# Performance work log

Measured on AMD Instinct MI355X. Metric: run time of the kernel, lower is better.

Reference implementation:

```python
import jax, jax.numpy as jnp
import numpy as np

D_MODEL = 1024
N_HEAD = 16
SEG = 256
HEAD_DIM = D_MODEL // N_HEAD  # 64; only used as softmax scale (module never splits heads)
SCALE = 1.0 / (HEAD_DIM ** 0.5)


def setup_inputs() -> dict:
    key = jax.random.key(0)
    ks = jax.random.split(key, 9)
    B, L, D = 4, 4096, D_MODEL
    s = 1.0 / np.sqrt(D)
    x = jax.random.normal(ks[0], (B, L, D), dtype=jnp.float32)
    Wq = jax.random.uniform(ks[1], (D, D), jnp.float32, -s, s)
    bq = jax.random.uniform(ks[2], (D,), jnp.float32, -s, s)
    Wk = jax.random.uniform(ks[3], (D, D), jnp.float32, -s, s)
    bk = jax.random.uniform(ks[4], (D,), jnp.float32, -s, s)
    Wv = jax.random.uniform(ks[5], (D, D), jnp.float32, -s, s)
    bv = jax.random.uniform(ks[6], (D,), jnp.float32, -s, s)
    Wo = jax.random.uniform(ks[7], (D, D), jnp.float32, -s, s)
    bo = jax.random.uniform(ks[8], (D,), jnp.float32, -s, s)
    return {"x": x, "Wq": Wq, "bq": bq, "Wk": Wk, "bk": bk,
            "Wv": Wv, "bv": bv, "Wo": Wo, "bo": bo}


def reference(x, Wq, bq, Wk, bk, Wv, bv, Wo, bo):
    B, L, D = x.shape
    n_seg = L // SEG
    xs = x.reshape(B, n_seg, SEG, D)  # [B, n, S, D] block-diagonal segments

    # Local (per-segment) attention, batched over all segments at once.
    Q = jnp.einsum('bnsd,ed->bnse', xs, Wq) + bq
    K = jnp.einsum('bnsd,ed->bnse', xs, Wk) + bk
    V = jnp.einsum('bnsd,ed->bnse', xs, Wv) + bv
    scores = jnp.einsum('bnse,bnte->bnst', Q, K) * SCALE  # [B, n, S, S]
    attn = jax.nn.softmax(scores, axis=-1)
    local = jnp.einsum('bnst,bnte->bnse', attn, V)  # [B, n, S, D]

    # Global attention over segment summaries (first token of each segment).
    summ = xs[:, :, 0, :]  # [B, n, D]
    Qg = jnp.einsum('bnd,ed->bne', summ, Wq) + bq
    Kg = jnp.einsum('bnd,ed->bne', summ, Wk) + bk
    Vg = jnp.einsum('bnd,ed->bne', summ, Wv) + bv
    scores_g = jnp.einsum('bne,bme->bnm', Qg, Kg) * SCALE  # [B, n, n]
    attn_g = jax.nn.softmax(scores_g, axis=-1)
    global_out = jnp.einsum('bnm,bme->bne', attn_g, Vg)  # [B, n, D]

    # Broadcast each segment's global summary over its tokens and add.
    out = local + global_out[:, :, None, :]  # [B, n, S, D]
    out = out.reshape(B, L, D)
    return jnp.einsum('bld,ed->ble', out, Wo) + bo
```

## Files before the change

### kernel.cpp

```cpp
#include <hip/hip_runtime.h>
#include <hip/hip_bf16.h>
#include <stdint.h>

typedef unsigned short u16;
typedef __attribute__((ext_vector_type(8))) short s16x8;
typedef __attribute__((ext_vector_type(4))) short s16x4;
typedef __attribute__((ext_vector_type(4))) float f32x4;

__device__ __forceinline__ u16 f2bf(float f){
  uint32_t u = __builtin_bit_cast(uint32_t, f);
  u += 0x7FFFu + ((u >> 16) & 1u);
  return (u16)(u >> 16);
}
__device__ __forceinline__ float bf2f(u16 h){
  uint32_t u = ((uint32_t)h) << 16;
  return __builtin_bit_cast(float, u);
}
__device__ __forceinline__ void gl_lds16(const void* g, void* l){
  __builtin_amdgcn_global_load_lds((__attribute__((address_space(1))) void*)g,
                                   (__attribute__((address_space(3))) void*)l,
                                   16, 0, 0);
}

#define MROWS 16384
#define DMODEL 1024
#define NQKV 3072
#define NSEGS 64
#define O_XB    0u
#define O_WQKV  33554432u
#define O_WO    39845888u
#define O_BQKV  41943040u
#define O_QKV   41955328u
#define O_VT    142618624u
#define O_GOUT  176173056u
#define O_GPR   176435200u

__global__ __launch_bounds__(256) void pack_kernel(
    const float* __restrict__ x,
    const float* __restrict__ wq, const float* __restrict__ wk,
    const float* __restrict__ wv, const float* __restrict__ wo,
    const float* __restrict__ bq, const float* __restrict__ bk, const float* __restrict__ bv,
    u16* __restrict__ xb, u16* __restrict__ wqkvb, u16* __restrict__ wob,
    float* __restrict__ bqkv)
{
  const int stride = gridDim.x * 256;
  const int gid = blockIdx.x * 256 + threadIdx.x;
  if(gid < 3072)
    bqkv[gid] = (gid < 1024) ? bq[gid] : (gid < 2048 ? bk[gid - 1024] : bv[gid - 2048]);
  for(int q = gid; q < 4194304; q += stride){
    float4 v = *(const float4*)(x + (size_t)q * 4);
    ushort4 o; o.x = f2bf(v.x); o.y = f2bf(v.y); o.z = f2bf(v.z); o.w = f2bf(v.w);
    *(ushort4*)(xb + (size_t)q * 4) = o;
  }
  for(int q = gid; q < 786432; q += stride){
    int elem = q << 2;
    int m = elem >> 20;
    const float* s = (m == 0) ? wq : (m == 1 ? wk : wv);
    float4 v = *(const float4*)(s + (elem & 1048575));
    ushort4 o; o.x = f2bf(v.x); o.y = f2bf(v.y); o.z = f2bf(v.z); o.w = f2bf(v.w);
    *(ushort4*)(wqkvb + elem) = o;
  }
  for(int q = gid; q < 262144; q += stride){
    float4 v = *(const float4*)(wo + (size_t)q * 4);
    ushort4 o; o.x = f2bf(v.x); o.y = f2bf(v.y); o.z = f2bf(v.z); o.w = f2bf(v.w);
    *(ushort4*)(wob + (size_t)q * 4) = o;
  }
}

__global__ __launch_bounds__(512, 2) void gemm256_kernel(
    const u16* __restrict__ A, const u16* __restrict__ Bt,
    const float* __restrict__ bias, u16* __restrict__ Cv,
    u16* __restrict__ Vt, const int K, const int ldc, const int ncb)
{
  __shared__ char sm[131072];
  const int tid = threadIdx.x;
  const int wv = tid >> 6, lane = tid & 63;
  const int l15 = lane & 15, l4 = lane >> 4;
  const int wr = wv >> 2, wc = wv & 3;

  const int nwg = (int)gridDim.x;
  int bid = (int)blockIdx.x;
  bid = (bid & 7) * (nwg >> 3) + (bid >> 3);
  const int brow = (bid / ncb) << 8, bcol = (bid % ncb) << 8;

  int offA[8], offB[4];
#pragma unroll
  for(int m = 0; m < 8; ++m){
    int row = wr * 128 + m * 16 + l15;
    offA[m] = row * 64 + ((l4 ^ ((row >> 1) & 3)) << 4);
  }
#pragma unroll
  for(int n = 0; n < 4; ++n){
    int row = wc * 64 + n * 16 + l15;
    offB[n] = 16384 + row * 64 + ((l4 ^ ((row >> 1) & 3)) << 4);
  }

  const u16* srcA[2]; const u16* srcB[2]; int dstOff[2];
#pragma unroll
  for(int r = 0; r < 2; ++r){
    int off = r * 8192 + tid * 16;
    int row = off >> 6, g = (off >> 4) & 3;
    int gs = g ^ ((row >> 1) & 3);
    srcA[r] = A  + (size_t)(brow + row) * K + gs * 8;
    srcB[r] = Bt + (size_t)(bcol + row) * K + gs * 8;
    dstOff[r] = r * 8192 + wv * 1024;
  }

#define STAGE256(kt_, buf_) do{                                   \
    char* base_ = sm + (buf_) * 32768;                            \
    const int ko_ = (kt_) << 5;                                   \
    gl_lds16(srcA[0] + ko_, base_ + dstOff[0]);                   \
    gl_lds16(srcA[1] + ko_, base_ + dstOff[1]);                   \
    gl_lds16(srcB[0] + ko_, base_ + 16384 + dstOff[0]);           \
    gl_lds16(srcB[1] + ko_, base_ + 16384 + dstOff[1]);           \
  }while(0)

  const f32x4 fz = {0.f, 0.f, 0.f, 0.f};
  f32x4 acc[8][4];
#pragma unroll
  for(int m = 0; m < 8; ++m)
#pragma unroll
    for(int n = 0; n < 4; ++n) acc[m][n] = fz;

  const int nkt = K >> 5;
  STAGE256(0, 0); STAGE256(1, 1); STAGE256(2, 2);

  for(int kt = 0; kt < nkt; ++kt){
    const int rem = nkt - 1 - kt;
    if(rem >= 2)      asm volatile("s_waitcnt vmcnt(8)" ::: "memory");
    else if(rem == 1) asm volatile("s_waitcnt vmcnt(4)" ::: "memory");
    else              asm volatile("s_waitcnt vmcnt(0)" ::: "memory");
    __builtin_amdgcn_s_barrier();
    asm volatile("" ::: "memory");
    if(kt + 3 < nkt) STAGE256(kt + 3, (kt + 3) & 3);

    char* cb = sm + (kt & 3) * 32768;
    s16x8 b[4], a[4];
#pragma unroll
    for(int n = 0; n < 4; ++n) b[n] = *(const s16x8*)(cb + offB[n]);
#pragma unroll
    for(int m = 0; m < 4; ++m) a[m] = *(const s16x8*)(cb + offA[m]);
    __builtin_amdgcn_s_setprio(1);
#pragma unroll
    for(int m = 0; m < 4; ++m)
#pragma unroll
      for(int n = 0; n < 4; ++n)
        acc[m][n] = __builtin_amdgcn_mfma_f32_16x16x32_bf16(a[m], b[n], acc[m][n], 0, 0, 0);
    __builtin_amdgcn_s_setprio(0);
#pragma unroll
    for(int m = 0; m < 4; ++m) a[m] = *(const s16x8*)(cb + offA[m + 4]);
    __builtin_amdgcn_s_setprio(1);
#pragma unroll
    for(int m = 0; m < 4; ++m)
#pragma unroll
      for(int n = 0; n < 4; ++n)
        acc[m + 4][n] = __builtin_amdgcn_mfma_f32_16x16x32_bf16(a[m], b[n], acc[m + 4][n], 0, 0, 0);
    __builtin_amdgcn_s_setprio(0);
  }
#undef STAGE256

  float bvv[4];
#pragma unroll
  for(int n = 0; n < 4; ++n) bvv[n] = bias[bcol + wc * 64 + n * 16 + l15];

  if(bcol < 2048){
#pragma unroll
    for(int m = 0; m < 8; ++m)
#pragma unroll
      for(int n = 0; n < 4; ++n)
#pragma unroll
        for(int r = 0; r < 4; ++r){
          const int row = brow + wr * 128 + m * 16 + (l4 << 2) + r;
          const int col = bcol + wc * 64 + n * 16 + l15;
          Cv[(size_t)row * ldc + col] = f2bf(acc[m][n][r] + bvv[n]);
        }
  } else {
    __syncthreads();
    char* wbase = sm + wv * 16384;
    const int swzW = (l15 & 7) << 4;
#pragma unroll
    for(int n = 0; n < 4; ++n)
#pragma unroll
      for(int m = 0; m < 8; ++m){
        s16x4 pk;
#pragma unroll
        for(int r = 0; r < 4; ++r) pk[r] = (short)f2bf(acc[m][n][r] + bvv[n]);
        const int eL = n * 16 + l15;
        const int tB = (m * 16 + (l4 << 2)) * 2;
        *(s16x4*)(wbase + ((eL * 256 + tB) ^ swzW)) = pk;
      }
    asm volatile("s_waitcnt lgkmcnt(0)" ::: "memory");
    const int seg = brow >> 8;
    const int e0  = bcol - 2048 + wc * 64;
    const int c = lane & 15, eSub = lane >> 4;
#pragma unroll
    for(int i = 0; i < 16; ++i){
      const int eL = i * 4 + eSub;
      s16x8 vvv = *(const s16x8*)(wbase + ((eL * 256 + c * 16) ^ ((eL & 7) << 4)));
      *(s16x8*)(Vt + (size_t)seg * 262144 + (size_t)(e0 + eL) * 256 + wr * 128 + c * 8) = vvv;
    }
  }
}

__global__ __launch_bounds__(512, 4) void gemm128_kernel(
    const u16* __restrict__ A, const u16* __restrict__ Bt,
    const float* __restrict__ bias, float* __restrict__ C,
    const int K, const int ldc, const int ncb)
{
  __shared__ char sm[73728];
  const int tid = threadIdx.x;
  const int wv = tid >> 6, lane = tid & 63;
  const int l15 = lane & 15, l4 = lane >> 4;
  const int wr = wv >> 2, wc = wv & 3;

  const int nwg = (int)gridDim.x;
  int bid = (int)blockIdx.x;
  bid = (bid & 7) * (nwg >> 3) + (bid >> 3);
  const int brow = (bid / ncb) << 8, bcol = (bid % ncb) << 7;

  int offA[8], offB[2];
#pragma unroll
  for(int m = 0; m < 8; ++m){
    int row = wr * 128 + m * 16 + l15;
    offA[m] = row * 64 + ((l4 ^ ((row >> 1) & 3)) << 4);
  }
#pragma unroll
  for(int n = 0; n < 2; ++n){
    int row = wc * 32 + n * 16 + l15;
    offB[n] = 16384 + row * 64 + ((l4 ^ ((row >> 1) & 3)) << 4);
  }

  const u16* srcA[2]; const u16* srcB; int dstOff[2];
#pragma unroll
  for(int r = 0; r < 2; ++r){
    int off = r * 8192 + tid * 16;
    int row = off >> 6, g = (off >> 4) & 3;
    int gs = g ^ ((row >> 1) & 3);
    srcA[r] = A + (size_t)(brow + row) * K + gs * 8;
    dstOff[r] = r * 8192 + wv * 1024;
  }
  {
    int off = tid * 16;
    int row = off >> 6, g = (off >> 4) & 3;
    int gs = g ^ ((row >> 1) & 3);
    srcB = Bt + (size_t)(bcol + row) * K + gs * 8;
  }

#define STAGE128(kt_, buf_) do{                                   \
    char* base_ = sm + (buf_) * 24576;                            \
    const int ko_ = (kt_) << 5;                                   \
    gl_lds16(srcA[0] + ko_, base_ + dstOff[0]);                   \
    gl_lds16(srcA[1] + ko_, base_ + dstOff[1]);                   \
    gl_lds16(srcB + ko_, base_ + 16384 + wv * 1024);              \
  }while(0)

  const f32x4 fz = {0.f, 0.f, 0.f, 0.f};
  f32x4 acc[8][2];
#pragma unroll
  for(int m = 0; m < 8; ++m)
#pragma unroll
    for(int n = 0; n < 2; ++n) acc[m][n] = fz;

  const int nkt = K >> 5;
  STAGE128(0, 0); STAGE128(1, 1);
  int cur = 0;
  for(int kt = 0; kt < nkt; ++kt){
    if(kt + 1 < nkt) asm volatile("s_waitcnt vmcnt(3)" ::: "memory");
    else             asm volatile("s_waitcnt vmcnt(0)" ::: "memory");
    __builtin_amdgcn_s_barrier();
    asm volatile("" ::: "memory");
    if(kt + 2 < nkt){
      int nb = cur + 2; if(nb >= 3) nb -= 3;
      STAGE128(kt + 2, nb);
    }
    char* cb = sm + cur * 24576;
    s16x8 b[2], a[4];
#pragma unroll
    for(int n = 0; n < 2; ++n) b[n] = *(const s16x8*)(cb + offB[n]);
#pragma unroll
    for(int m = 0; m < 4; ++m) a[m] = *(const s16x8*)(cb + offA[m]);
    __builtin_amdgcn_s_setprio(1);
#pragma unroll
    for(int m = 0; m < 4; ++m)
#pragma unroll
      for(int n = 0; n < 2; ++n)
        acc[m][n] = __builtin_amdgcn_mfma_f32_16x16x32_bf16(a[m], b[n], acc[m][n], 0, 0, 0);
    __builtin_amdgcn_s_setprio(0);
#pragma unroll
    for(int m = 0; m < 4; ++m) a[m] = *(const s16x8*)(cb + offA[m + 4]);
    __builtin_amdgcn_s_setprio(1);
#pragma unroll
    for(int m = 0; m < 4; ++m)
#pragma unroll
      for(int n = 0; n < 2; ++n)
        acc[m + 4][n] = __builtin_amdgcn_mfma_f32_16x16x32_bf16(a[m], b[n], acc[m + 4][n], 0, 0, 0);
    __builtin_amdgcn_s_setprio(0);
    if(++cur == 3) cur = 0;
  }
#undef STAGE128

  float bvv[2];
#pragma unroll
  for(int n = 0; n < 2; ++n) bvv[n] = bias[bcol + wc * 32 + n * 16 + l15];
#pragma unroll
  for(int m = 0; m < 8; ++m)
#pragma unroll
    for(int n = 0; n < 2; ++n)
#pragma unroll
      for(int r = 0; r < 4; ++r){
        const int row = brow + wr * 128 + m * 16 + (l4 << 2) + r;
        const int col = bcol + wc * 32 + n * 16 + l15;
        C[(size_t)row * ldc + col] = acc[m][n][r] + bvv[n];
      }
}

__global__ __launch_bounds__(256) void gscore_kernel(
    const u16* __restrict__ QKV, float* __restrict__ gpr)
{
  __shared__ float sc[16];
  const int b = blockIdx.x >> 4, i = blockIdx.x & 15;
  const int tid = threadIdx.x;
  const int j = tid >> 4, slice = tid & 15;
  const u16* qp = QKV + (size_t)(b * 16 + i) * 256 * NQKV + slice * 64;
  const u16* kp = QKV + (size_t)(b * 16 + j) * 256 * NQKV + 1024 + slice * 64;
  float acc = 0.f;
#pragma unroll
  for(int c = 0; c < 8; ++c){
    s16x8 qv = *(const s16x8*)(qp + c * 8);
    s16x8 kv = *(const s16x8*)(kp + c * 8);
#pragma unroll
    for(int e = 0; e < 8; ++e) acc += bf2f((u16)qv[e]) * bf2f((u16)kv[e]);
  }
#pragma unroll
  for(int off = 8; off >= 1; off >>= 1) acc += __shfl_xor(acc, off, 64);
  if(slice == 0) sc[j] = acc * 0.125f;
  __syncthreads();
  if(tid < 16){
    float v = sc[tid];
    float m = v;
#pragma unroll
    for(int off = 8; off >= 1; off >>= 1) m = fmaxf(m, __shfl_xor(m, off, 64));
    float p = __expf(v - m);
    float s = p;
#pragma unroll
    for(int off = 8; off >= 1; off >>= 1) s += __shfl_xor(s, off, 64);
    gpr[(size_t)b * 256 + i * 16 + tid] = p / s;
  }
}

__global__ __launch_bounds__(256) void gpv_kernel(
    const u16* __restrict__ Vt, const float* __restrict__ gpr,
    float* __restrict__ gout)
{
  __shared__ float spr[256];
  const int b = blockIdx.x >> 4, ch = blockIdx.x & 15;
  const int tid = threadIdx.x;
  spr[tid] = gpr[(size_t)b * 256 + tid];
  __syncthreads();
  const int e = (ch << 6) + (tid & 63);
  const int ng = tid >> 6;
  const u16* vp = Vt + (size_t)(b * 16) * 262144 + (size_t)e * 256;
  float o0 = 0.f, o1 = 0.f, o2 = 0.f, o3 = 0.f;
#pragma unroll
  for(int m = 0; m < 16; ++m){
    float v = bf2f(vp[(size_t)m * 262144]);
    o0 += spr[(ng * 4 + 0) * 16 + m] * v;
    o1 += spr[(ng * 4 + 1) * 16 + m] * v;
    o2 += spr[(ng * 4 + 2) * 16 + m] * v;
    o3 += spr[(ng * 4 + 3) * 16 + m] * v;
  }
  gout[((size_t)b * 16 + ng * 4 + 0) * 1024 + e] = o0;
  gout[((size_t)b * 16 + ng * 4 + 1) * 1024 + e] = o1;
  gout[((size_t)b * 16 + ng * 4 + 2) * 1024 + e] = o2;
  gout[((size_t)b * 16 + ng * 4 + 3) * 1024 + e] = o3;
}

__global__ __launch_bounds__(512, 2) void attn_local_kernel(
    const u16* __restrict__ QKV, const u16* __restrict__ Vt,
    const float* __restrict__ gout, u16* __restrict__ AO)
{
  __shared__ char sm[131072];
  float* smax = (float*)(sm + 32768);
  float* ssum = (float*)(sm + 33792);
  const int tid = threadIdx.x;
  const int wv = tid >> 6, lane = tid & 63;
  const int l15 = lane & 15, l4 = lane >> 4;
  const int wr = wv >> 2, wc = wv & 3;
  int bid = (int)blockIdx.x;
  bid = (bid & 7) * 32 + (bid >> 3);
  const int seg = bid >> 2, rt = bid & 3;
  const int r0 = rt << 6;
  const size_t segQ = (size_t)seg * 256 * NQKV;

  const int offq = wv * 1024 + lane * 16;
  const int dstQ = wv * 1024;
  const int qrow = offq >> 7;
  const int qgs  = ((offq >> 4) & 7) ^ (qrow & 7);
  const u16* qsrc = QKV + segQ + (size_t)(r0 + qrow) * NQKV + qgs * 8;
  const u16* ksrc[4];
  const u16* vsrc[4];
#pragma unroll
  for(int c = 0; c < 4; ++c){
    int off = c * 8192 + offq;
    int row = off >> 7;
    int gs  = ((off >> 4) & 7) ^ (row & 7);
    ksrc[c] = QKV + segQ + (size_t)row * NQKV + 1024 + gs * 8;
    vsrc[c] = Vt + (size_t)seg * 262144 + (size_t)row * 256 + gs * 8;
  }

#define STAGE_P1(d0_, base_) do{                                        \
    gl_lds16(qsrc + (d0_), sm + (base_) + dstQ);                        \
    _Pragma("unroll")                                                   \
    for(int c_ = 0; c_ < 4; ++c_)                                       \
      gl_lds16(ksrc[c_] + (d0_), sm + (base_) + 8192 + c_ * 8192 + dstQ); \
  }while(0)
#define STAGE_V(j_, vb_) do{                                            \
    const int vo_ = ((j_) >> 2) * 65536 + ((j_) & 3) * 64;              \
    _Pragma("unroll")                                                   \
    for(int c_ = 0; c_ < 4; ++c_)                                       \
      gl_lds16(vsrc[c_] + vo_, sm + 32768 + (vb_) * 32768 + c_ * 8192 + dstQ); \
  }while(0)

  int aOff[2][2], bOff[4][2];
#pragma unroll
  for(int m = 0; m < 2; ++m){
    int row = wr * 32 + m * 16 + l15;
#pragma unroll
    for(int kk = 0; kk < 2; ++kk)
      aOff[m][kk] = row * 128 + ((kk * 64 + l4 * 16) ^ ((row & 7) << 4));
  }
#pragma unroll
  for(int n = 0; n < 4; ++n){
    int row = wc * 64 + n * 16 + l15;
#pragma unroll
    for(int kk = 0; kk < 2; ++kk)
      bOff[n][kk] = 8192 + row * 128 + ((kk * 64 + l4 * 16) ^ ((row & 7) << 4));
  }

  const f32x4 fz = {0.f, 0.f, 0.f, 0.f};
  f32x4 acc1[2][4];
#pragma unroll
  for(int m = 0; m < 2; ++m)
#pragma unroll
    for(int n = 0; n < 4; ++n) acc1[m][n] = fz;

  STAGE_P1(0, 0); STAGE_P1(64, 40960);
  asm volatile("s_waitcnt vmcnt(5)" ::: "memory");
  __builtin_amdgcn_s_barrier();
  asm volatile("" ::: "memory");
  int cur = 0;
  for(int dt = 0; dt < 16; ++dt){
    const int base = cur * 40960;
    if(dt + 2 < 16){
      int nb = cur + 2; if(nb >= 3) nb -= 3;
      STAGE_P1((dt + 2) << 6, nb * 40960);
    }
    s16x8 a[2][2], b[4][2];
#pragma unroll
    for(int m = 0; m < 2; ++m)
#pragma unroll
      for(int kk = 0; kk < 2; ++kk) a[m][kk] = *(const s16x8*)(sm + base + aOff[m][kk]);
#pragma unroll
    for(int n = 0; n < 4; ++n)
#pragma unroll
      for(int kk = 0; kk < 2; ++kk) b[n][kk] = *(const s16x8*)(sm + base + bOff[n][kk]);
    __builtin_amdgcn_s_setprio(1);
#pragma unroll
    for(int kk = 0; kk < 2; ++kk)
#pragma unroll
      for(int m = 0; m < 2; ++m)
#pragma unroll
        for(int n = 0; n < 4; ++n)
          acc1[m][n] = __builtin_amdgcn_mfma_f32_16x16x32_bf16(a[m][kk], b[n][kk], acc1[m][n], 0, 0, 0);
    __builtin_amdgcn_s_setprio(0);
    if(dt + 2 < 16) asm volatile("s_waitcnt vmcnt(5) lgkmcnt(0)" ::: "memory");
    else            asm volatile("s_waitcnt vmcnt(0) lgkmcnt(0)" ::: "memory");
    __builtin_amdgcn_s_barrier();
    asm volatile("" ::: "memory");
    if(++cur == 3) cur = 0;
  }

  const float CE = 0.18033688011112042f;
#pragma unroll
  for(int m = 0; m < 2; ++m)
#pragma unroll
    for(int r = 0; r < 4; ++r){
      float v = -1e30f;
#pragma unroll
      for(int n = 0; n < 4; ++n) v = fmaxf(v, acc1[m][n][r]);
#pragma unroll
      for(int off = 8; off >= 1; off >>= 1) v = fmaxf(v, __shfl_xor(v, off, 64));
      if(l15 == 0) smax[wc * 64 + wr * 32 + m * 16 + (l4 << 2) + r] = v;
    }
  asm volatile("s_waitcnt lgkmcnt(0)" ::: "memory");
  __builtin_amdgcn_s_barrier();
  asm volatile("" ::: "memory");
#pragma unroll
  for(int m = 0; m < 2; ++m)
#pragma unroll
    for(int r = 0; r < 4; ++r){
      const int idx = wr * 32 + m * 16 + (l4 << 2) + r;
      const float g = fmaxf(fmaxf(smax[idx], smax[64 + idx]),
                            fmaxf(smax[128 + idx], smax[192 + idx]));
      float s = 0.f;
#pragma unroll
      for(int n = 0; n < 4; ++n){
        float p = exp2f((acc1[m][n][r] - g) * CE);
        acc1[m][n][r] = p;
        s += p;
      }
#pragma unroll
      for(int off = 8; off >= 1; off >>= 1) s += __shfl_xor(s, off, 64);
      if(l15 == 0) ssum[wc * 64 + idx] = s;
    }
  asm volatile("s_waitcnt lgkmcnt(0)" ::: "memory");
  __builtin_amdgcn_s_barrier();
  asm volatile("" ::: "memory");
  float inv2[2][4];
#pragma unroll
  for(int m = 0; m < 2; ++m)
#pragma unroll
    for(int r = 0; r < 4; ++r){
      const int idx = wr * 32 + m * 16 + (l4 << 2) + r;
      inv2[m][r] = 1.f / (ssum[idx] + ssum[64 + idx] + ssum[128 + idx] + ssum[192 + idx]);
    }
#pragma unroll
  for(int m = 0; m < 2; ++m)
#pragma unroll
    for(int n = 0; n < 4; ++n)
#pragma unroll
      for(int r = 0; r < 4; ++r){
        const int rr = wr * 32 + m * 16 + (l4 << 2) + r;
        const int t  = wc * 64 + n * 16 + l15;
        *(u16*)(sm + rr * 512 + ((t << 1) ^ ((rr & 7) << 4))) = f2bf(acc1[m][n][r] * inv2[m][r]);
      }
  asm volatile("s_waitcnt lgkmcnt(0)" ::: "memory");
  __builtin_amdgcn_s_barrier();
  asm volatile("" ::: "memory");

  int prow[2], pswz[2];
#pragma unroll
  for(int m = 0; m < 2; ++m){
    int row = wr * 32 + m * 16 + l15;
    prow[m] = row * 512;
    pswz[m] = (row & 7) << 4;
  }
  int vOff[4][2];
#pragma unroll
  for(int n = 0; n < 4; ++n){
    int row = wc * 64 + n * 16 + l15;
#pragma unroll
    for(int kk = 0; kk < 2; ++kk)
      vOff[n][kk] = row * 128 + ((kk * 64 + l4 * 16) ^ ((row & 7) << 4));
  }

  STAGE_V(0, 0); STAGE_V(1, 1);
  asm volatile("s_waitcnt vmcnt(4)" ::: "memory");
  __builtin_amdgcn_s_barrier();
  asm volatile("" ::: "memory");
  f32x4 acc2[2][4];
  int cv = 0;
  for(int j = 0; j < 16; ++j){
    const int ts = j & 3, ns = j >> 2;
    if(ts == 0){
#pragma unroll
      for(int m = 0; m < 2; ++m)
#pragma unroll
        for(int n = 0; n < 4; ++n) acc2[m][n] = fz;
    }
    if(j + 2 < 16){
      int nb = cv + 2; if(nb >= 3) nb -= 3;
      STAGE_V(j + 2, nb);
    }
    char* vbase = sm + 32768 + cv * 32768;
    s16x8 a[2][2], b[4][2];
#pragma unroll
    for(int m = 0; m < 2; ++m)
#pragma unroll
      for(int kk = 0; kk < 2; ++kk)
        a[m][kk] = *(const s16x8*)(sm + prow[m] + (((ts << 7) + (kk << 6) + (l4 << 4)) ^ pswz[m]));
#pragma unroll
    for(int n = 0; n < 4; ++n)
#pragma unroll
      for(int kk = 0; kk < 2; ++kk) b[n][kk] = *(const s16x8*)(vbase + vOff[n][kk]);
    __builtin_amdgcn_s_setprio(1);
#pragma unroll
    for(int kk = 0; kk < 2; ++kk)
#pragma unroll
      for(int m = 0; m < 2; ++m)
#pragma unroll
        for(int n = 0; n < 4; ++n)
          acc2[m][n] = __builtin_amdgcn_mfma_f32_16x16x32_bf16(a[m][kk], b[n][kk], acc2[m][n], 0, 0, 0);
    __builtin_amdgcn_s_setprio(0);
    if(j + 2 < 16) asm volatile("s_waitcnt vmcnt(4) lgkmcnt(0)" ::: "memory");
    else           asm volatile("s_waitcnt vmcnt(0) lgkmcnt(0)" ::: "memory");
    __builtin_amdgcn_s_barrier();
    asm volatile("" ::: "memory");
    if(++cv == 3) cv = 0;

    if(ts == 3){
      float gv[4];
#pragma unroll
      for(int n = 0; n < 4; ++n)
        gv[n] = gout[(size_t)seg * 1024 + ns * 256 + wc * 64 + n * 16 + l15];
#pragma unroll
      for(int m = 0; m < 2; ++m)
#pragma unroll
        for(int n = 0; n < 4; ++n)
#pragma unroll
          for(int r = 0; r < 4; ++r){
            const int row = r0 + wr * 32 + m * 16 + (l4 << 2) + r;
            const int e   = ns * 256 + wc * 64 + n * 16 + l15;
            AO[((size_t)seg * 256 + row) * 1024 + e] = f2bf(acc2[m][n][r] + gv[n]);
          }
    }
  }
#undef STAGE_P1
#undef STAGE_V
}

extern "C" void kernel_launch(void* const* d_in, const int* in_sizes, int n_in,
                              void* d_out, int out_size, void* d_ws, size_t ws_size,
                              hipStream_t stream)
{
  const float* x  = (const float*)d_in[0];
  const float* Wq = (const float*)d_in[1];
  const float* bq = (const float*)d_in[2];
  const float* Wk = (const float*)d_in[3];
  const float* bk = (const float*)d_in[4];
  const float* Wv = (const float*)d_in[5];
  const float* bv = (const float*)d_in[6];
  const float* Wo = (const float*)d_in[7];
  const float* bo = (const float*)d_in[8];

  char* ws = (char*)d_ws;
  u16*   xb    = (u16*)(ws + O_XB);
  u16*   wqkvb = (u16*)(ws + O_WQKV);
  u16*   wob   = (u16*)(ws + O_WO);
  float* bqkv  = (float*)(ws + O_BQKV);
  u16*   qkv   = (u16*)(ws + O_QKV);
  u16*   vt    = (u16*)(ws + O_VT);
  float* gout  = (float*)(ws + O_GOUT);
  float* gpr   = (float*)(ws + O_GPR);
  u16*   ao    = xb;

  pack_kernel<<<4096, 256, 0, stream>>>(x, Wq, Wk, Wv, Wo, bq, bk, bv, xb, wqkvb, wob, bqkv);
  gemm256_kernel<<<dim3((NQKV / 256) * (MROWS / 256)), 512, 0, stream>>>(
      xb, wqkvb, bqkv, qkv, vt, DMODEL, NQKV, NQKV / 256);
  gscore_kernel<<<64, 256, 0, stream>>>(qkv, gpr);
  gpv_kernel<<<64, 256, 0, stream>>>(vt, gpr, gout);
  attn_local_kernel<<<256, 512, 0, stream>>>(qkv, vt, gout, ao);
  gemm128_kernel<<<dim3((DMODEL / 128) * (MROWS / 256)), 512, 0, stream>>>(
      ao, wob, bo, (float*)d_out, DMODEL, DMODEL, DMODEL / 128);
}
```

Baseline: 212.2 us.

## Halve attention row tile to 32 rows, double blocks, cut LDS for occupancy

```diff
diff --git a/kernel.cpp b/kernel.cpp
--- a/kernel.cpp
+++ b/kernel.cpp
@@ -375,25 +375,24 @@
   gout[((size_t)b * 16 + ng * 4 + 3) * 1024 + e] = o3;
 }
 
-__global__ __launch_bounds__(512, 2) void attn_local_kernel(
+__global__ __launch_bounds__(512, 4) void attn_local_kernel(
     const u16* __restrict__ QKV, const u16* __restrict__ Vt,
     const float* __restrict__ gout, u16* __restrict__ AO)
 {
-  __shared__ char sm[131072];
-  float* smax = (float*)(sm + 32768);
-  float* ssum = (float*)(sm + 33792);
+  __shared__ char sm[81920];
+  float* smax = (float*)(sm + 16384);
+  float* ssum = (float*)(sm + 17408);
   const int tid = threadIdx.x;
   const int wv = tid >> 6, lane = tid & 63;
   const int l15 = lane & 15, l4 = lane >> 4;
   const int wr = wv >> 2, wc = wv & 3;
   int bid = (int)blockIdx.x;
-  bid = (bid & 7) * 32 + (bid >> 3);
-  const int seg = bid >> 2, rt = bid & 3;
-  const int r0 = rt << 6;
+  bid = (bid & 7) * 64 + (bid >> 3);
+  const int seg = bid >> 3, rt = bid & 7;
+  const int r0 = rt << 5;
   const size_t segQ = (size_t)seg * 256 * NQKV;
 
-  const int offq = wv * 1024 + lane * 16;
-  const int dstQ = wv * 1024;
+  const int offq = tid * 16;
   const int qrow = offq >> 7;
   const int qgs  = ((offq >> 4) & 7) ^ (qrow & 7);
   const u16* qsrc = QKV + segQ + (size_t)(r0 + qrow) * NQKV + qgs * 8;
@@ -401,216 +400,189 @@
   const u16* vsrc[4];
 #pragma unroll
   for(int c = 0; c < 4; ++c){
-    int off = c * 8192 + offq;
+    int off = c * 8192 + tid * 16;
     int row = off >> 7;
     int gs  = ((off >> 4) & 7) ^ (row & 7);
     ksrc[c] = QKV + segQ + (size_t)row * NQKV + 1024 + gs * 8;
     vsrc[c] = Vt + (size_t)seg * 262144 + (size_t)row * 256 + gs * 8;
   }
-
-#define STAGE_P1(d0_, base_) do{                                        \
-    gl_lds16(qsrc + (d0_), sm + (base_) + dstQ);                        \
-    _Pragma("unroll")                                                   \
-    for(int c_ = 0; c_ < 4; ++c_)                                       \
-      gl_lds16(ksrc[c_] + (d0_), sm + (base_) + 8192 + c_ * 8192 + dstQ); \
+  const int dstW = wv * 1024;
+
+#define STAGE_P1(d0_, buf_) do{                                          \
+    char* b_ = sm + (buf_) * 36864;                                      \
+    if(wv < 4) gl_lds16(qsrc + (d0_), b_ + dstW);                        \
+    _Pragma("unroll")                                                    \
+    for(int c_ = 0; c_ < 4; ++c_)                                        \
+      gl_lds16(ksrc[c_] + (d0_), b_ + 4096 + c_ * 8192 + dstW);          \
   }while(0)
-#define STAGE_V(j_, vb_) do{                                            \
-    const int vo_ = ((j_) >> 2) * 65536 + ((j_) & 3) * 64;              \
-    _Pragma("unroll")                                                   \
-    for(int c_ = 0; c_ < 4; ++c_)                                       \
-      gl_lds16(vsrc[c_] + vo_, sm + 32768 + (vb_) * 32768 + c_ * 8192 + dstQ); \
+#define STAGE_V(j_, vb_) do{                                             \
+    const int vo_ = ((j_) >> 2) * 65536 + ((j_) & 3) * 64;               \
+    _Pragma("unroll")                                                    \
+    for(int c_ = 0; c_ < 4; ++c_)                                        \
+      gl_lds16(vsrc[c_] + vo_, sm + 16384 + (vb_) * 32768 + c_ * 8192 + dstW); \
   }while(0)
 
-  int aOff[2][2], bOff[4][2];
-#pragma unroll
-  for(int m = 0; m < 2; ++m){
-    int row = wr * 32 + m * 16 + l15;
+  int aOff[2], bOff[4][2];
+  {
+    int row = wr * 16 + l15;
 #pragma unroll
     for(int kk = 0; kk < 2; ++kk)
-      aOff[m][kk] = row * 128 + ((kk * 64 + l4 * 16) ^ ((row & 7) << 4));
+      aOff[kk] = row * 128 + ((kk * 64 + l4 * 16) ^ ((row & 7) << 4));
   }
 #pragma unroll
   for(int n = 0; n < 4; ++n){
     int row = wc * 64 + n * 16 + l15;
 #pragma unroll
     for(int kk = 0; kk < 2; ++kk)
-      bOff[n][kk] = 8192 + row * 128 + ((kk * 64 + l4 * 16) ^ ((row & 7) << 4));
+      bOff[n][kk] = 4096 + row * 128 + ((kk * 64 + l4 * 16) ^ ((row & 7) << 4));
   }
 
   const f32x4 fz = {0.f, 0.f, 0.f, 0.f};
-  f32x4 acc1[2][4];
-#pragma unroll
-  for(int m = 0; m < 2; ++m)
-#pragma unroll
-    for(int n = 0; n < 4; ++n) acc1[m][n] = fz;
-
-  STAGE_P1(0, 0); STAGE_P1(64, 40960);
-  asm volatile("s_waitcnt vmcnt(5)" ::: "memory");
+  f32x4 acc1[4];
+#pragma unroll
+  for(int n = 0; n < 4; ++n) acc1[n] = fz;
+
+  STAGE_P1(0, 0);
+  for(int dt = 0; dt < 16; ++dt){
+    asm volatile("s_waitcnt vmcnt(0)" ::: "memory");
+    __builtin_amdgcn_s_barrier();
+    asm volatile("" ::: "memory");
+    if(dt + 1 < 16) STAGE_P1((dt + 1) << 6, (dt + 1) & 1);
+    char* cb = sm + (dt & 1) * 36864;
+    s16x8 a[2], b[4][2];
+#pragma unroll
+    for(int kk = 0; kk < 2; ++kk) a[kk] = *(const s16x8*)(cb + aOff[kk]);
+#pragma unroll
+    for(int n = 0; n < 4; ++n)
+#pragma unroll
+      for(int kk = 0; kk < 2; ++kk) b[n][kk] = *(const s16x8*)(cb + bOff[n][kk]);
+    asm volatile("s_waitcnt lgkmcnt(0)" ::: "memory");
+    __builtin_amdgcn_s_setprio(1);
+#pragma unroll
+    for(int kk = 0; kk < 2; ++kk)
+#pragma unroll
+      for(int n = 0; n < 4; ++n)
+        acc1[n] = __builtin_amdgcn_mfma_f32_16x16x32_bf16(a[kk], b[n][kk], acc1[n], 0, 0, 0);
+    __builtin_amdgcn_s_setprio(0);
+  }
   __builtin_amdgcn_s_barrier();
   asm volatile("" ::: "memory");
-  int cur = 0;
-  for(int dt = 0; dt < 16; ++dt){
-    const int base = cur * 40960;
-    if(dt + 2 < 16){
-      int nb = cur + 2; if(nb >= 3) nb -= 3;
-      STAGE_P1((dt + 2) << 6, nb * 40960);
+
+  const float CE = 0.18033688011112042f;
+#pragma unroll
+  for(int r = 0; r < 4; ++r){
+    float v = -1e30f;
+#pragma unroll
+    for(int n = 0; n < 4; ++n) v = fmaxf(v, acc1[n][r]);
+#pragma unroll
+    for(int off = 8; off >= 1; off >>= 1) v = fmaxf(v, __shfl_xor(v, off, 64));
+    if(l15 == 0) smax[wc * 32 + wr * 16 + (l4 << 2) + r] = v;
+  }
+  asm volatile("s_waitcnt lgkmcnt(0)" ::: "memory");
+  __builtin_amdgcn_s_barrier();
+  asm volatile("" ::: "memory");
+  float inv2[4];
+#pragma unroll
+  for(int r = 0; r < 4; ++r){
+    const int idx = wr * 16 + (l4 << 2) + r;
+    const float g = fmaxf(fmaxf(smax[idx], smax[32 + idx]),
+                          fmaxf(smax[64 + idx], smax[96 + idx]));
+    float s = 0.f;
+#pragma unroll
+    for(int n = 0; n < 4; ++n){
+      float p = exp2f((acc1[n][r] - g) * CE);
+      acc1[n][r] = p;
+      s += p;
     }
-    s16x8 a[2][2], b[4][2];
-#pragma unroll
-    for(int m = 0; m < 2; ++m)
-#pragma unroll
-      for(int kk = 0; kk < 2; ++kk) a[m][kk] = *(const s16x8*)(sm + base + aOff[m][kk]);
-#pragma unroll
-    for(int n = 0; n < 4; ++n)
-#pragma unroll
-      for(int kk = 0; kk < 2; ++kk) b[n][kk] = *(const s16x8*)(sm + base + bOff[n][kk]);
-    __builtin_amdgcn_s_setprio(1);
-#pragma unroll
-    for(int kk = 0; kk < 2; ++kk)
-#pragma unroll
-      for(int m = 0; m < 2; ++m)
-#pragma unroll
-        for(int n = 0; n < 4; ++n)
-          acc1[m][n] = __builtin_amdgcn_mfma_f32_16x16x32_bf16(a[m][kk], b[n][kk], acc1[m][n], 0, 0, 0);
-    __builtin_amdgcn_s_setprio(0);
-    if(dt + 2 < 16) asm volatile("s_waitcnt vmcnt(5) lgkmcnt(0)" ::: "memory");
-    else            asm volatile("s_waitcnt vmcnt(0) lgkmcnt(0)" ::: "memory");
-    __builtin_amdgcn_s_barrier();
-    asm volatile("" ::: "memory");
-    if(++cur == 3) cur = 0;
-  }
-
-  const float CE = 0.18033688011112042f;
-#pragma unroll
-  for(int m = 0; m < 2; ++m)
+#pragma unroll
+    for(int off = 8; off >= 1; off >>= 1) s += __shfl_xor(s, off, 64);
+    if(l15 == 0) ssum[wc * 32 + idx] = s;
+  }
+  asm volatile("s_waitcnt lgkmcnt(0)" ::: "memory");
+  __builtin_amdgcn_s_barrier();
+  asm volatile("" ::: "memory");
+#pragma unroll
+  for(int r = 0; r < 4; ++r){
+    const int idx = wr * 16 + (l4 << 2) + r;
+    inv2[r] = 1.f / (ssum[idx] + ssum[32 + idx] + ssum[64 + idx] + ssum[96 + idx]);
+  }
+#pragma unroll
+  for(int n = 0; n < 4; ++n)
 #pragma unroll
     for(int r = 0; r < 4; ++r){
-      float v = -1e30f;
-#pragma unroll
-      for(int n = 0; n < 4; ++n) v = fmaxf(v, acc1[m][n][r]);
-#pragma unroll
-      for(int off = 8; off >= 1; off >>= 1) v = fmaxf(v, __shfl_xor(v, off, 64));
-      if(l15 == 0) smax[wc * 64 + wr * 32 + m * 16 + (l4 << 2) + r] = v;
+      const int rr = wr * 16 + (l4 << 2) + r;
+      const int t  = wc * 64 + n * 16 + l15;
+      *(u16*)(sm + rr * 512 + ((t << 1) ^ ((rr & 7) << 4))) = f2bf(acc1[n][r] * inv2[r]);
     }
   asm volatile("s_waitcnt lgkmcnt(0)" ::: "memory");
   __builtin_amdgcn_s_barrier();
   asm volatile("" ::: "memory");
-#pragma unroll
-  for(int m = 0; m < 2; ++m)
-#pragma unroll
-    for(int r = 0; r < 4; ++r){
-      const int idx = wr * 32 + m * 16 + (l4 << 2) + r;
-      const float g = fmaxf(fmaxf(smax[idx], smax[64 + idx]),
-                            fmaxf(smax[128 + idx], smax[192 + idx]));
-      float s = 0.f;
-#pragma unroll
-      for(int n = 0; n < 4; ++n){
-        float p = exp2f((acc1[m][n][r] - g) * CE);
-        acc1[m][n][r] = p;
-        s += p;
-      }
-#pragma unroll
-      for(int off = 8; off >= 1; off >>= 1) s += __shfl_xor(s, off, 64);
-      if(l15 == 0) ssum[wc * 64 + idx] = s;
-    }
-  asm volatile("s_waitcnt lgkmcnt(0)" ::: "memory");
-  __builtin_amdgcn_s_barrier();
-  asm volatile("" ::: "memory");
-  float inv2[2][4];
-#pragma unroll
-  for(int m = 0; m < 2; ++m)
-#pragma unroll
-    for(int r = 0; r < 4; ++r){
-      const int idx = wr * 32 + m * 16 + (l4 << 2) + r;
-      inv2[m][r] = 1.f / (ssum[idx] + ssum[64 + idx] + ssum[128 + idx] + ssum[192 + idx]);
-    }
-#pragma unroll
-  for(int m = 0; m < 2; ++m)
-#pragma unroll
-    for(int n = 0; n < 4; ++n)
-#pragma unroll
-      for(int r = 0; r < 4; ++r){
-        const int rr = wr * 32 + m * 16 + (l4 << 2) + r;
-        const int t  = wc * 64 + n * 16 + l15;
-        *(u16*)(sm + rr * 512 + ((t << 1) ^ ((rr & 7) << 4))) = f2bf(acc1[m][n][r] * inv2[m][r]);
-      }
-  asm volatile("s_waitcnt lgkmcnt(0)" ::: "memory");
-  __builtin_amdgcn_s_barrier();
-  asm volatile("" ::: "memory");
 
   int prow[2], pswz[2];
 #pragma unroll
   for(int m = 0; m < 2; ++m){
-    int row = wr * 32 + m * 16 + l15;
+    int row = m * 16 + l15;
     prow[m] = row * 512;
     pswz[m] = (row & 7) << 4;
   }
-  int vOff[4][2];
-#pragma unroll
-  for(int n = 0; n < 4; ++n){
-    int row = wc * 64 + n * 16 + l15;
+  int vOff[2][2];
+#pragma unroll
+  for(int n = 0; n < 2; ++n){
+    int row = wv * 32 + n * 16 + l15;
 #pragma unroll
     for(int kk = 0; kk < 2; ++kk)
       vOff[n][kk] = row * 128 + ((kk * 64 + l4 * 16) ^ ((row & 7) << 4));
   }
 
-  STAGE_V(0, 0); STAGE_V(1, 1);
-  asm volatile("s_waitcnt vmcnt(4)" ::: "memory");
-  __builtin_amdgcn_s_barrier();
-  asm volatile("" ::: "memory");
-  f32x4 acc2[2][4];
-  int cv = 0;
+  STAGE_V(0, 0);
+  f32x4 acc2[2][2];
   for(int j = 0; j < 16; ++j){
     const int ts = j & 3, ns = j >> 2;
+    asm volatile("s_waitcnt vmcnt(0)" ::: "memory");
+    __builtin_amdgcn_s_barrier();
+    asm volatile("" ::: "memory");
+    if(j + 1 < 16) STAGE_V(j + 1, (j + 1) & 1);
     if(ts == 0){
 #pragma unroll
       for(int m = 0; m < 2; ++m)
 #pragma unroll
-        for(int n = 0; n < 4; ++n) acc2[m][n] = fz;
+        for(int n = 0; n < 2; ++n) acc2[m][n] = fz;
     }
-    if(j + 2 < 16){
-      int nb = cv + 2; if(nb >= 3) nb -= 3;
-      STAGE_V(j + 2, nb);
-    }
-    char* vbase = sm + 32768 + cv * 32768;
-    s16x8 a[2][2], b[4][2];
+    char* vbase = sm + 16384 + (j & 1) * 32768;
+    s16x8 a[2][2], b[2][2];
 #pragma unroll
     for(int m = 0; m < 2; ++m)
 #pragma unroll
       for(int kk = 0; kk < 2; ++kk)
         a[m][kk] = *(const s16x8*)(sm + prow[m] + (((ts << 7) + (kk << 6) + (l4 << 4)) ^ pswz[m]));
 #pragma unroll
-    for(int n = 0; n < 4; ++n)
+    for(int n = 0; n < 2; ++n)
 #pragma unroll
       for(int kk = 0; kk < 2; ++kk) b[n][kk] = *(const s16x8*)(vbase + vOff[n][kk]);
+    asm volatile("s_waitcnt lgkmcnt(0)" ::: "memory");
     __builtin_amdgcn_s_setprio(1);
 #pragma unroll
     for(int kk = 0; kk < 2; ++kk)
 #pragma unroll
       for(int m = 0; m < 2; ++m)
 #pragma unroll
-        for(int n = 0; n < 4; ++n)
+        for(int n = 0; n < 2; ++n)
           acc2[m][n] = __builtin_amdgcn_mfma_f32_16x16x32_bf16(a[m][kk], b[n][kk], acc2[m][n], 0, 0, 0);
     __builtin_amdgcn_s_setprio(0);
-    if(j + 2 < 16) asm volatile("s_waitcnt vmcnt(4) lgkmcnt(0)" ::: "memory");
-    else           asm volatile("s_waitcnt vmcnt(0) lgkmcnt(0)" ::: "memory");
-    __builtin_amdgcn_s_barrier();
-    asm volatile("" ::: "memory");
-    if(++cv == 3) cv = 0;
 
     if(ts == 3){
-      float gv[4];
-#pragma unroll
-      for(int n = 0; n < 4; ++n)
-        gv[n] = gout[(size_t)seg * 1024 + ns * 256 + wc * 64 + n * 16 + l15];
+      float gv[2];
+#pragma unroll
+      for(int n = 0; n < 2; ++n)
+        gv[n] = gout[(size_t)seg * 1024 + ns * 256 + wv * 32 + n * 16 + l15];
 #pragma unroll
       for(int m = 0; m < 2; ++m)
 #pragma unroll
-        for(int n = 0; n < 4; ++n)
+        for(int n = 0; n < 2; ++n)
 #pragma unroll
           for(int r = 0; r < 4; ++r){
-            const int row = r0 + wr * 32 + m * 16 + (l4 << 2) + r;
-            const int e   = ns * 256 + wc * 64 + n * 16 + l15;
+            const int row = r0 + m * 16 + (l4 << 2) + r;
+            const int e   = ns * 256 + wv * 32 + n * 16 + l15;
             AO[((size_t)seg * 256 + row) * 1024 + e] = f2bf(acc2[m][n][r] + gv[n]);
           }
     }
@@ -649,7 +621,7 @@
       xb, wqkvb, bqkv, qkv, vt, DMODEL, NQKV, NQKV / 256);
   gscore_kernel<<<64, 256, 0, stream>>>(qkv, gpr);
   gpv_kernel<<<64, 256, 0, stream>>>(vt, gpr, gout);
-  attn_local_kernel<<<256, 512, 0, stream>>>(qkv, vt, gout, ao);
+  attn_local_kernel<<<512, 512, 0, stream>>>(qkv, vt, gout, ao);
   gemm128_kernel<<<dim3((DMODEL / 128) * (MROWS / 256)), 512, 0, stream>>>(
       ao, wob, bo, (float*)d_out, DMODEL, DMODEL, DMODEL / 128);
 }
```

Result: no change. 214.7 us (+1.2%).
